# Optimization experiments

Hardware: AMD Instinct MI355X
Metric: run time of the kernel (lower is better)

## Reference

```python
import jax, jax.numpy as jnp
import numpy as np

B, N, E = 32, 128, 16384
D, H, O, A = 72, 72, 72, 4   # n_input, n_hidden, n_output, n_node_attr
C_WEIGHT = 1.0
EPS = 1e-5  # BatchNorm1d default eps


def setup_inputs() -> dict:
    key = jax.random.key(0)
    ks = jax.random.split(key, 16)
    rn = lambda k, shp, s=0.05: jax.random.normal(k, shp, jnp.float32) * s
    return {
        "h": jax.random.normal(ks[0], (B, N, D), jnp.float32),
        "x": jax.random.normal(ks[1], (B, N, 4), jnp.float32),
        "edgei": jax.random.randint(ks[2], (B, E), 0, N),
        "edgej": jax.random.randint(ks[3], (B, E), 0, N),
        "node_attr": jax.random.normal(ks[4], (B, N, A), jnp.float32),
        # phi_e: Linear(2D+2 -> H, no bias), BN, ReLU, Linear(H->H), ReLU
        "We1": rn(ks[5], (2 * D + 2, H)),
        "g1": jnp.ones((H,), jnp.float32), "b1": jnp.zeros((H,), jnp.float32),
        "We2": rn(ks[6], (H, H)), "be2": jnp.zeros((H,), jnp.float32),
        # phi_m: Linear(H->1), Sigmoid
        "Wm": rn(ks[7], (H, 1)), "bm": jnp.zeros((1,), jnp.float32),
        # phi_x: Linear(H->H), ReLU, Linear(H->1, no bias, tiny init)
        "Wx1": rn(ks[8], (H, H)), "bx1": jnp.zeros((H,), jnp.float32),
        "Wx2": rn(ks[9], (H, 1), 0.001),
        # phi_h: Linear(H+D+A -> H), BN, ReLU, Linear(H->O)
        "Wh1": rn(ks[10], (H + D + A, H)), "bh1": jnp.zeros((H,), jnp.float32),
        "gh": jnp.ones((H,), jnp.float32), "bh": jnp.zeros((H,), jnp.float32),
        "Wh2": rn(ks[11], (H, O)), "bh2": jnp.zeros((O,), jnp.float32),
    }


def _psi(p):
    return jnp.sign(p) * jnp.log1p(jnp.abs(p))


def _normsq4(p):  # Minkowski norm: p0^2 - p1^2 - p2^2 - p3^2
    psq = p * p
    return 2.0 * psq[..., 0] - psq.sum(axis=-1)


def _dotsq4(p, q):  # Minkowski inner product
    pq = p * q
    return 2.0 * pq[..., 0] - pq.sum(axis=-1)


def _batchnorm(z, g, b):  # training-mode BatchNorm1d over flattened batch dim
    mu = z.mean(axis=0)
    var = z.var(axis=0)
    return (z - mu) * jax.lax.rsqrt(var + EPS) * g + b


_seg_sum = jax.vmap(lambda d, s: jax.ops.segment_sum(d, s, num_segments=N))


def reference(h, x, edgei, edgej, node_attr,
              We1, g1, b1, We2, be2, Wm, bm,
              Wx1, bx1, Wx2, Wh1, bh1, gh, bh, Wh2, bh2):
    # gather edge endpoint features (equiv. to torch.gather along dim 1)
    xi = jnp.take_along_axis(x, edgei[:, :, None], axis=1)    # [B,E,4]
    xj = jnp.take_along_axis(x, edgej[:, :, None], axis=1)
    hi = jnp.take_along_axis(h, edgei[:, :, None], axis=1)    # [B,E,D]
    hj = jnp.take_along_axis(h, edgej[:, :, None], axis=1)
    x_diff = xi - xj
    norms = _psi(_normsq4(x_diff))[..., None]                 # [B,E,1]
    dots = _psi(_dotsq4(xi, xj))[..., None]                   # [B,E,1]

    # m_model: phi_e then sigmoid gate phi_m
    feat = jnp.concatenate([hi, hj, norms, dots], axis=-1)    # [B,E,2D+2]
    z = feat.reshape(-1, 2 * D + 2) @ We1
    z = jax.nn.relu(_batchnorm(z, g1, b1))
    z = jax.nn.relu(z @ We2 + be2)
    m = z.reshape(B, E, H)
    m = m * jax.nn.sigmoid(m @ Wm + bm)                       # gated messages

    # x_model: equivariant coordinate update (segment mean over edges)
    gate = jax.nn.relu(m @ Wx1 + bx1) @ Wx2                   # [B,E,1]
    trans = jnp.clip(x_diff * gate, -100.0, 100.0)
    agg = _seg_sum(trans, edgei)                              # [B,N,4]
    cnt = _seg_sum(jnp.ones_like(trans), edgei)
    x_out = x + (agg / jnp.maximum(cnt, 1.0)) * C_WEIGHT

    # h_model: segment sum of messages, node MLP, residual
    magg = _seg_sum(m, edgei)                                 # [B,N,H]
    hin = jnp.concatenate([h, magg, node_attr], axis=-1).reshape(-1, H + D + A)
    z2 = hin @ Wh1 + bh1
    z2 = jax.nn.relu(_batchnorm(z2, gh, bh))
    z2 = z2 @ Wh2 + bh2
    h_out = h + z2.reshape(B, N, O)

    return (h_out, x_out, m)
```

## Files before the change

kernel.cpp:

```cpp
#include <hip/hip_runtime.h>

#define BB 32
#define NN 128
#define EE 16384
#define ROWS_E (BB*EE)
#define ROWS_N (BB*NN)
#define EPS_BN 1e-5f

#define XOUT_OFF (ROWS_N*72)
#define M_OFF    (XOUT_OFF + ROWS_N*4)

#define ST1_OFF 0
#define ST2_OFF 512
#define AGG_OFF 1024
#define CNT_OFF (AGG_OFF + ROWS_N*4)
#define MAGG_OFF (CNT_OFF + ROWS_N)
#define Z2_OFF (MAGG_OFF + ROWS_N*72)
#define ZERO_FLOATS Z2_OFF
#define WB_OFF (Z2_OFF + ROWS_N*72)

#define WE1T_OFF 0
#define WE2T_OFF 13440
#define WX1T_OFF 21760
#define WH1T_OFF 30080
#define WH2T_OFF 43520
#define WB_TOTAL 51840

typedef __attribute__((ext_vector_type(8))) short short8;
typedef __attribute__((ext_vector_type(4))) float f32x4;

__device__ __forceinline__ float psi_f(float p) {
    return copysignf(log1pf(fabsf(p)), p);
}
__device__ __forceinline__ unsigned short f2bf(float f) {
    union { float f; unsigned u; } v; v.f = f;
    unsigned r = v.u + 0x7fffu + ((v.u >> 16) & 1u);
    return (unsigned short)(r >> 16);
}
__device__ __forceinline__ unsigned pk(float a, float b) {
    return (unsigned)f2bf(a) | ((unsigned)f2bf(b) << 16);
}

__global__ void k_prep(const float* __restrict__ We1, const float* __restrict__ We2,
                       const float* __restrict__ Wx1, const float* __restrict__ Wh1,
                       const float* __restrict__ Wh2, unsigned short* __restrict__ wb)
{
    int idx = blockIdx.x * 256 + threadIdx.x;
    if (idx >= WB_TOTAL) return;
    const float* src; int off, n, k, K;
    if (idx < WE2T_OFF)      { off = idx;            n = off/168; k = off%168; src = We1; K = 146; }
    else if (idx < WH1T_OFF && idx >= WX1T_OFF) { off = idx - WX1T_OFF; n = off/104; k = off%104; src = Wx1; K = 72; }
    else if (idx < WX1T_OFF) { off = idx - WE2T_OFF; n = off/104; k = off%104; src = We2; K = 72; }
    else if (idx < WH2T_OFF) { off = idx - WH1T_OFF; n = off/168; k = off%168; src = Wh1; K = 148; }
    else                     { off = idx - WH2T_OFF; n = off/104; k = off%104; src = Wh2; K = 72; }
    float v = (n < 72 && k < K) ? src[k * 72 + n] : 0.f;
    wb[idx] = f2bf(v);
}

__global__ __launch_bounds__(256, 4) void k_edge_gemm1(
    const float* __restrict__ h, const float* __restrict__ x,
    const int* __restrict__ ei, const int* __restrict__ ej,
    const unsigned short* __restrict__ We1t, float* __restrict__ z1,
    float* __restrict__ st)
{
    __shared__ unsigned short At[128 * 160];
    int tid = threadIdx.x;
    int rl = tid >> 1, half = tid & 1;
    int row = blockIdx.x * 128 + rl;
    int b = row >> 14;
    int i = ei[row], j = ej[row];
    int node = half ? j : i;
    const float4* hp = (const float4*)(h + (size_t)(b * 128 + node) * 72);
    uint2* arow = (uint2*)(&At[rl * 160 + half * 72]);
    #pragma unroll
    for (int q = 0; q < 18; q++) {
        float4 v = hp[q];
        arow[q] = make_uint2(pk(v.x, v.y), pk(v.z, v.w));
    }
    if (half == 0) {
        float4 xi = *(const float4*)(x + (size_t)(b * 128 + i) * 4);
        float4 xj = *(const float4*)(x + (size_t)(b * 128 + j) * 4);
        float d0 = xi.x - xj.x, d1 = xi.y - xj.y, d2 = xi.z - xj.z, d3 = xi.w - xj.w;
        float nrm = d0*d0 - d1*d1 - d2*d2 - d3*d3;
        float dot = xi.x*xj.x - xi.y*xj.y - xi.z*xj.z - xi.w*xj.w;
        *(unsigned*)(&At[rl * 160 + 144]) = pk(psi_f(nrm), psi_f(dot));
        unsigned* tp = (unsigned*)(&At[rl * 160 + 146]);
        tp[0] = 0u; tp[1] = 0u; tp[2] = 0u;
    } else {
        unsigned* tp = (unsigned*)(&At[rl * 160 + 152]);
        tp[0] = 0u; tp[1] = 0u; tp[2] = 0u; tp[3] = 0u;
    }

    int wv = tid >> 6, lane = tid & 63, c = lane & 15, quad = lane >> 4;
    f32x4 acc[2][5] = {};
    for (int kc = 0; kc < 5; kc++) {
        int k0 = kc * 32 + quad * 8;
        short8 a0 = *(const short8*)(&At[(wv * 32 + c) * 160 + k0]);
        short8 a1 = *(const short8*)(&At[(wv * 32 + 16 + c) * 160 + k0]);
        #pragma unroll
        for (int ct = 0; ct < 5; ct++) {
            short8 bf = *(const short8*)(&We1t[(ct * 16 + c) * 168 + k0]);
            acc[0][ct] = __builtin_amdgcn_mfma_f32_16x16x32_bf16(a0, bf, acc[0][ct], 0, 0, 0);
            acc[1][ct] = __builtin_amdgcn_mfma_f32_16x16x32_bf16(a1, bf, acc[1][ct], 0, 0, 0);
        }
    }
    size_t rbase = (size_t)blockIdx.x * 128 + wv * 32 + quad * 4;
    float* sredw = (float*)(&At[wv * 32 * 160]);
    #pragma unroll
    for (int ct = 0; ct < 5; ct++) {
        int col = ct * 16 + c;
        float s = 0.f, q = 0.f;
        #pragma unroll
        for (int rt = 0; rt < 2; rt++) {
            float* op = z1 + (rbase + rt * 16) * 72 + col;
            #pragma unroll
            for (int r = 0; r < 4; r++) {
                float v = acc[rt][ct][r];
                if (col < 72) op[(size_t)r * 72] = v;
                s += v; q += v * v;
            }
        }
        s += __shfl_xor(s, 16); s += __shfl_xor(s, 32);
        q += __shfl_xor(q, 16); q += __shfl_xor(q, 32);
        if (lane < 16 && col < 72) { sredw[col] = s; sredw[72 + col] = q; }
    }
    __syncthreads();
    if (tid < 144) {
        const float* a = (const float*)At;
        atomicAdd(&st[tid], a[tid] + a[2560 + tid] + a[5120 + tid] + a[7680 + tid]);
    }
}

__global__ void k_finalize(float* __restrict__ st, float inv_rows)
{
    int c = threadIdx.x;
    if (c < 72) {
        float mean = st[c] * inv_rows;
        float var  = st[72 + c] * inv_rows - mean * mean;
        st[144 + c] = mean;
        st[216 + c] = rsqrtf(var + EPS_BN);
    }
}

__global__ __launch_bounds__(256, 6) void k_edge_main(
    const float* __restrict__ x, const int* __restrict__ ei, const int* __restrict__ ej,
    const float* __restrict__ st1, const float* __restrict__ g1, const float* __restrict__ b1,
    const float* __restrict__ be2, const float* __restrict__ Wm, const float* __restrict__ bm,
    const float* __restrict__ bx1, const float* __restrict__ Wx2,
    const unsigned short* __restrict__ We2t, const unsigned short* __restrict__ Wx1t,
    float* __restrict__ m, float* __restrict__ agg, float* __restrict__ cnt)
{
    __shared__ unsigned short Zt[128 * 104];
    __shared__ float g2buf[128];
    int tid = threadIdx.x;
    int rl = tid >> 1, half = tid & 1;
    size_t row = (size_t)blockIdx.x * 128 + rl;
    const float* mean = st1 + 144;
    const float* inv  = st1 + 216;
    const float4* zp = (const float4*)(m + row * 72) + half * 9;
    uint2* arow = (uint2*)(&Zt[rl * 104 + half * 36]);
    #pragma unroll
    for (int q = 0; q < 9; q++) {
        int k = half * 36 + q * 4;
        float4 v = zp[q];
        float a0 = fmaxf((v.x - mean[k  ]) * inv[k  ] * g1[k  ] + b1[k  ], 0.f);
        float a1 = fmaxf((v.y - mean[k+1]) * inv[k+1] * g1[k+1] + b1[k+1], 0.f);
        float a2 = fmaxf((v.z - mean[k+2]) * inv[k+2] * g1[k+2] + b1[k+2], 0.f);
        float a3 = fmaxf((v.w - mean[k+3]) * inv[k+3] * g1[k+3] + b1[k+3], 0.f);
        arow[q] = make_uint2(pk(a0, a1), pk(a2, a3));
    }
    uint2* prow = (uint2*)(&Zt[rl * 104]);
    #pragma unroll
    for (int q = 0; q < 4; q++) prow[18 + half * 4 + q] = make_uint2(0u, 0u);

    int wv = tid >> 6, lane = tid & 63, c = lane & 15, quad = lane >> 4;
    f32x4 acc2[2][5] = {};
    for (int kc = 0; kc < 3; kc++) {
        int k0 = kc * 32 + quad * 8;
        short8 a0 = *(const short8*)(&Zt[(wv * 32 + c) * 104 + k0]);
        short8 a1 = *(const short8*)(&Zt[(wv * 32 + 16 + c) * 104 + k0]);
        #pragma unroll
        for (int ct = 0; ct < 5; ct++) {
            short8 bf = *(const short8*)(&We2t[(ct * 16 + c) * 104 + k0]);
            acc2[0][ct] = __builtin_amdgcn_mfma_f32_16x16x32_bf16(a0, bf, acc2[0][ct], 0, 0, 0);
            acc2[1][ct] = __builtin_amdgcn_mfma_f32_16x16x32_bf16(a1, bf, acc2[1][ct], 0, 0, 0);
        }
    }
    float part[2][4] = {};
    float bm0 = bm[0];
    #pragma unroll
    for (int ct = 0; ct < 5; ct++) {
        int col = ct * 16 + c;
        float bias = (col < 72) ? be2[col] : 0.f;
        float wm   = (col < 72) ? Wm[col]  : 0.f;
        #pragma unroll
        for (int rt = 0; rt < 2; rt++)
            #pragma unroll
            for (int r = 0; r < 4; r++) {
                float t = fmaxf(acc2[rt][ct][r] + bias, 0.f);
                acc2[rt][ct][r] = t;
                part[rt][r] += t * wm;
            }
    }
    float sg[2][4];
    #pragma unroll
    for (int rt = 0; rt < 2; rt++)
        #pragma unroll
        for (int r = 0; r < 4; r++) {
            float s = part[rt][r];
            s += __shfl_xor(s, 1); s += __shfl_xor(s, 2);
            s += __shfl_xor(s, 4); s += __shfl_xor(s, 8);
            sg[rt][r] = 1.f / (1.f + expf(-(s + bm0)));
        }
    size_t rbase = (size_t)blockIdx.x * 128 + wv * 32 + quad * 4;
    #pragma unroll
    for (int rt = 0; rt < 2; rt++)
        #pragma unroll
        for (int ct = 0; ct < 5; ct++) {
            int col = ct * 16 + c;
            #pragma unroll
            for (int r = 0; r < 4; r++) {
                float mv = acc2[rt][ct][r] * sg[rt][r];
                int lrow = wv * 32 + rt * 16 + quad * 4 + r;
                Zt[lrow * 104 + col] = f2bf(mv);
                if (col < 72) m[(rbase + rt * 16 + r) * 72 + col] = mv;
            }
        }
    f32x4 acc3[2][5] = {};
    for (int kc = 0; kc < 3; kc++) {
        int k0 = kc * 32 + quad * 8;
        short8 a0 = *(const short8*)(&Zt[(wv * 32 + c) * 104 + k0]);
        short8 a1 = *(const short8*)(&Zt[(wv * 32 + 16 + c) * 104 + k0]);
        #pragma unroll
        for (int ct = 0; ct < 5; ct++) {
            short8 bf = *(const short8*)(&Wx1t[(ct * 16 + c) * 104 + k0]);
            acc3[0][ct] = __builtin_amdgcn_mfma_f32_16x16x32_bf16(a0, bf, acc3[0][ct], 0, 0, 0);
            acc3[1][ct] = __builtin_amdgcn_mfma_f32_16x16x32_bf16(a1, bf, acc3[1][ct], 0, 0, 0);
        }
    }
    float part3[2][4] = {};
    #pragma unroll
    for (int ct = 0; ct < 5; ct++) {
        int col = ct * 16 + c;
        float bias = (col < 72) ? bx1[col] : 0.f;
        float wx   = (col < 72) ? Wx2[col] : 0.f;
        #pragma unroll
        for (int rt = 0; rt < 2; rt++)
            #pragma unroll
            for (int r = 0; r < 4; r++)
                part3[rt][r] += fmaxf(acc3[rt][ct][r] + bias, 0.f) * wx;
    }
    #pragma unroll
    for (int rt = 0; rt < 2; rt++)
        #pragma unroll
        for (int r = 0; r < 4; r++) {
            float s = part3[rt][r];
            s += __shfl_xor(s, 1); s += __shfl_xor(s, 2);
            s += __shfl_xor(s, 4); s += __shfl_xor(s, 8);
            if (c == 0) g2buf[wv * 32 + rt * 16 + quad * 4 + r] = s;
        }
    __syncthreads();
    if (tid < 128) {
        size_t erow = (size_t)blockIdx.x * 128 + tid;
        int b = (int)(erow >> 14);
        int i2 = ei[erow], j2 = ej[erow];
        float g2 = g2buf[tid];
        float4 xi = *(const float4*)(x + (size_t)(b * 128 + i2) * 4);
        float4 xj = *(const float4*)(x + (size_t)(b * 128 + j2) * 4);
        float t0 = fminf(fmaxf((xi.x - xj.x) * g2, -100.f), 100.f);
        float t1 = fminf(fmaxf((xi.y - xj.y) * g2, -100.f), 100.f);
        float t2 = fminf(fmaxf((xi.z - xj.z) * g2, -100.f), 100.f);
        float t3 = fminf(fmaxf((xi.w - xj.w) * g2, -100.f), 100.f);
        float* ap = agg + (size_t)(b * 128 + i2) * 4;
        atomicAdd(ap + 0, t0); atomicAdd(ap + 1, t1);
        atomicAdd(ap + 2, t2); atomicAdd(ap + 3, t3);
        atomicAdd(cnt + (size_t)(b * 128 + i2), 1.f);
    }
}

__global__ __launch_bounds__(256, 4) void k_magg(
    const float* __restrict__ m, const int* __restrict__ ei, float* __restrict__ magg)
{
    __shared__ float accum[128 * 72];
    int tid = threadIdx.x;
    for (int q = tid; q < 9216; q += 256) accum[q] = 0.f;
    __syncthreads();
    int b = blockIdx.x >> 4, chunk = blockIdx.x & 15;
    int wv = tid >> 6, lane = tid & 63;
    int ebase = b * 16384 + chunk * 1024;
    for (int e = wv; e < 1024; e += 4) {
        int erow = ebase + e;
        int node = ei[erow];
        const float* mr = m + (size_t)erow * 72;
        atomicAdd(&accum[node * 72 + lane], mr[lane]);
        if (lane < 8) atomicAdd(&accum[node * 72 + 64 + lane], mr[64 + lane]);
    }
    __syncthreads();
    float* mg = magg + (size_t)b * 9216;
    for (int q = tid; q < 9216; q += 256) atomicAdd(&mg[q], accum[q]);
}

__global__ __launch_bounds__(256) void k_node_gemm1(
    const float* __restrict__ h, const float* __restrict__ node_attr,
    const float* __restrict__ magg, const unsigned short* __restrict__ Wh1t,
    const float* __restrict__ bh1, float* __restrict__ z2, float* __restrict__ st)
{
    __shared__ unsigned short At[128 * 168];
    __shared__ unsigned short Wt[80 * 168];
    __shared__ float sred[4][144];
    int tid = threadIdx.x;
    {
        const uint4* s = (const uint4*)Wh1t; uint4* d = (uint4*)Wt;
        for (int q = tid; q < 1680; q += 256) d[q] = s[q];
    }
    int rl = tid >> 1, half = tid & 1;
    size_t row = (size_t)blockIdx.x * 128 + rl;
    const float4* sp = (const float4*)((half ? magg : h) + row * 72);
    uint2* arow = (uint2*)(&At[rl * 168 + half * 72]);
    #pragma unroll
    for (int q = 0; q < 18; q++) {
        float4 v = sp[q];
        arow[q] = make_uint2(pk(v.x, v.y), pk(v.z, v.w));
    }
    if (half) {
        float4 na = *(const float4*)(node_attr + row * 4);
        *(unsigned*)(&At[rl * 168 + 144]) = pk(na.x, na.y);
        *(unsigned*)(&At[rl * 168 + 146]) = pk(na.z, na.w);
        unsigned* tailp = (unsigned*)(&At[rl * 168 + 148]);
        #pragma unroll
        for (int q = 0; q < 10; q++) tailp[q] = 0u;
    }
    __syncthreads();

    int wv = tid >> 6, lane = tid & 63, c = lane & 15, quad = lane >> 4;
    f32x4 acc[2][5] = {};
    for (int kc = 0; kc < 5; kc++) {
        int k0 = kc * 32 + quad * 8;
        short8 a0 = *(const short8*)(&At[(wv * 32 + c) * 168 + k0]);
        short8 a1 = *(const short8*)(&At[(wv * 32 + 16 + c) * 168 + k0]);
        #pragma unroll
        for (int ct = 0; ct < 5; ct++) {
            short8 bf = *(const short8*)(&Wt[(ct * 16 + c) * 168 + k0]);
            acc[0][ct] = __builtin_amdgcn_mfma_f32_16x16x32_bf16(a0, bf, acc[0][ct], 0, 0, 0);
            acc[1][ct] = __builtin_amdgcn_mfma_f32_16x16x32_bf16(a1, bf, acc[1][ct], 0, 0, 0);
        }
    }
    size_t rbase = (size_t)blockIdx.x * 128 + wv * 32 + quad * 4;
    #pragma unroll
    for (int ct = 0; ct < 5; ct++) {
        int col = ct * 16 + c;
        float bias = (col < 72) ? bh1[col] : 0.f;
        float s = 0.f, q = 0.f;
        #pragma unroll
        for (int rt = 0; rt < 2; rt++) {
            float* op = z2 + (rbase + rt * 16) * 72 + col;
            #pragma unroll
            for (int r = 0; r < 4; r++) {
                float v = acc[rt][ct][r] + bias;
                if (col < 72) op[(size_t)r * 72] = v;
                s += v; q += v * v;
            }
        }
        s += __shfl_xor(s, 16); s += __shfl_xor(s, 32);
        q += __shfl_xor(q, 16); q += __shfl_xor(q, 32);
        if (lane < 16 && col < 72) { sred[wv][col] = s; sred[wv][72 + col] = q; }
    }
    __syncthreads();
    if (tid < 144)
        atomicAdd(&st[tid], sred[0][tid] + sred[1][tid] + sred[2][tid] + sred[3][tid]);
}

__global__ __launch_bounds__(256) void k_node_final(
    const float* __restrict__ h, const float* __restrict__ x,
    const float* __restrict__ z2, const float* __restrict__ st2,
    const float* __restrict__ gh, const float* __restrict__ bh,
    const unsigned short* __restrict__ Wh2t, const float* __restrict__ bh2,
    const float* __restrict__ agg, const float* __restrict__ cnt,
    float* __restrict__ hout, float* __restrict__ xout)
{
    __shared__ unsigned short Zt[128 * 104];
    __shared__ unsigned short Wt[80 * 104];
    int tid = threadIdx.x;
    {
        const uint4* s = (const uint4*)Wh2t; uint4* d = (uint4*)Wt;
        for (int q = tid; q < 1040; q += 256) d[q] = s[q];
    }
    int rl = tid >> 1, half = tid & 1;
    size_t row = (size_t)blockIdx.x * 128 + rl;
    const float* mean = st2 + 144;
    const float* inv  = st2 + 216;
    const float4* zp = (const float4*)(z2 + row * 72) + half * 9;
    uint2* arow = (uint2*)(&Zt[rl * 104 + half * 36]);
    #pragma unroll
    for (int q = 0; q < 9; q++) {
        int k = half * 36 + q * 4;
        float4 v = zp[q];
        float a0 = fmaxf((v.x - mean[k  ]) * inv[k  ] * gh[k  ] + bh[k  ], 0.f);
        float a1 = fmaxf((v.y - mean[k+1]) * inv[k+1] * gh[k+1] + bh[k+1], 0.f);
        float a2 = fmaxf((v.z - mean[k+2]) * inv[k+2] * gh[k+2] + bh[k+2], 0.f);
        float a3 = fmaxf((v.w - mean[k+3]) * inv[k+3] * gh[k+3] + bh[k+3], 0.f);
        arow[q] = make_uint2(pk(a0, a1), pk(a2, a3));
    }
    uint2* prow = (uint2*)(&Zt[rl * 104]);
    #pragma unroll
    for (int q = 0; q < 4; q++) prow[18 + half * 4 + q] = make_uint2(0u, 0u);
    __syncthreads();

    int wv = tid >> 6, lane = tid & 63, c = lane & 15, quad = lane >> 4;
    f32x4 acc[2][5] = {};
    for (int kc = 0; kc < 3; kc++) {
        int k0 = kc * 32 + quad * 8;
        short8 a0 = *(const short8*)(&Zt[(wv * 32 + c) * 104 + k0]);
        short8 a1 = *(const short8*)(&Zt[(wv * 32 + 16 + c) * 104 + k0]);
        #pragma unroll
        for (int ct = 0; ct < 5; ct++) {
            short8 bf = *(const short8*)(&Wt[(ct * 16 + c) * 104 + k0]);
            acc[0][ct] = __builtin_amdgcn_mfma_f32_16x16x32_bf16(a0, bf, acc[0][ct], 0, 0, 0);
            acc[1][ct] = __builtin_amdgcn_mfma_f32_16x16x32_bf16(a1, bf, acc[1][ct], 0, 0, 0);
        }
    }
    size_t rbase = (size_t)blockIdx.x * 128 + wv * 32 + quad * 4;
    #pragma unroll
    for (int rt = 0; rt < 2; rt++)
        #pragma unroll
        for (int ct = 0; ct < 5; ct++) {
            int col = ct * 16 + c;
            if (col < 72) {
                float bias = bh2[col];
                #pragma unroll
                for (int r = 0; r < 4; r++) {
                    size_t gr = (rbase + rt * 16 + r);
                    hout[gr * 72 + col] = h[gr * 72 + col] + acc[rt][ct][r] + bias;
                }
            }
        }
    if (tid < 128) {
        size_t nrow = (size_t)blockIdx.x * 128 + tid;
        float cn = fmaxf(cnt[nrow], 1.f);
        float4 ag = *(const float4*)(agg + nrow * 4);
        float4 xv = *(const float4*)(x + nrow * 4);
        ((float4*)xout)[nrow] = make_float4(xv.x + ag.x / cn, xv.y + ag.y / cn,
                                            xv.z + ag.z / cn, xv.w + ag.w / cn);
    }
}

extern "C" void kernel_launch(void* const* d_in, const int* in_sizes, int n_in,
                              void* d_out, int out_size, void* d_ws, size_t ws_size,
                              hipStream_t stream)
{
    const float* h   = (const float*)d_in[0];
    const float* x   = (const float*)d_in[1];
    const int*   ei  = (const int*)d_in[2];
    const int*   ej  = (const int*)d_in[3];
    const float* na  = (const float*)d_in[4];
    const float* We1 = (const float*)d_in[5];
    const float* g1  = (const float*)d_in[6];
    const float* b1  = (const float*)d_in[7];
    const float* We2 = (const float*)d_in[8];
    const float* be2 = (const float*)d_in[9];
    const float* Wm  = (const float*)d_in[10];
    const float* bm  = (const float*)d_in[11];
    const float* Wx1 = (const float*)d_in[12];
    const float* bx1 = (const float*)d_in[13];
    const float* Wx2 = (const float*)d_in[14];
    const float* Wh1 = (const float*)d_in[15];
    const float* bh1 = (const float*)d_in[16];
    const float* gh  = (const float*)d_in[17];
    const float* bhp = (const float*)d_in[18];
    const float* Wh2 = (const float*)d_in[19];
    const float* bh2 = (const float*)d_in[20];

    float* out  = (float*)d_out;
    float* hout = out;
    float* xout = out + XOUT_OFF;
    float* m    = out + M_OFF;
    float* ws   = (float*)d_ws;
    float* st1  = ws + ST1_OFF;
    float* st2  = ws + ST2_OFF;
    float* agg  = ws + AGG_OFF;
    float* cnt  = ws + CNT_OFF;
    float* magg = ws + MAGG_OFF;
    float* z2   = ws + Z2_OFF;
    unsigned short* wb = (unsigned short*)(ws + WB_OFF);

    hipMemsetAsync(d_ws, 0, (size_t)ZERO_FLOATS * sizeof(float), stream);
    k_prep<<<(WB_TOTAL + 255) / 256, 256, 0, stream>>>(We1, We2, Wx1, Wh1, Wh2, wb);
    k_edge_gemm1<<<ROWS_E / 128, 256, 0, stream>>>(h, x, ei, ej, wb + WE1T_OFF, m, st1);
    k_finalize<<<1, 128, 0, stream>>>(st1, 1.0f / (float)ROWS_E);
    k_edge_main<<<ROWS_E / 128, 256, 0, stream>>>(x, ei, ej, st1, g1, b1, be2, Wm, bm,
                                                  bx1, Wx2, wb + WE2T_OFF, wb + WX1T_OFF,
                                                  m, agg, cnt);
    k_magg<<<512, 256, 0, stream>>>(m, ei, magg);
    k_node_gemm1<<<ROWS_N / 128, 256, 0, stream>>>(h, na, magg, wb + WH1T_OFF, bh1, z2, st2);
    k_finalize<<<1, 128, 0, stream>>>(st2, 1.0f / (float)ROWS_N);
    k_node_final<<<ROWS_N / 128, 256, 0, stream>>>(h, x, z2, st2, gh, bhp,
                                                   wb + WH2T_OFF, bh2, agg, cnt, hout, xout);
}
```

Measured before the change: 720.9 us.

## Recompute first edge GEMM in fused kernel instead of storing intermediate z1

```diff
diff --git a/kernel.cpp b/kernel.cpp
--- a/kernel.cpp
+++ b/kernel.cpp
@@ -57,16 +57,12 @@
     wb[idx] = f2bf(v);
 }
 
-__global__ __launch_bounds__(256, 4) void k_edge_gemm1(
-    const float* __restrict__ h, const float* __restrict__ x,
-    const int* __restrict__ ei, const int* __restrict__ ej,
-    const unsigned short* __restrict__ We1t, float* __restrict__ z1,
-    float* __restrict__ st)
-{
-    __shared__ unsigned short At[128 * 160];
-    int tid = threadIdx.x;
+__device__ __forceinline__ void stage_feat(
+    unsigned short* At, const float* __restrict__ h, const float* __restrict__ x,
+    const int* __restrict__ ei, const int* __restrict__ ej, int tid, int blk)
+{
     int rl = tid >> 1, half = tid & 1;
-    int row = blockIdx.x * 128 + rl;
+    int row = blk * 128 + rl;
     int b = row >> 14;
     int i = ei[row], j = ej[row];
     int node = half ? j : i;
@@ -90,6 +86,16 @@
         unsigned* tp = (unsigned*)(&At[rl * 160 + 152]);
         tp[0] = 0u; tp[1] = 0u; tp[2] = 0u; tp[3] = 0u;
     }
+}
+
+__global__ __launch_bounds__(256, 4) void k_edge_stats(
+    const float* __restrict__ h, const float* __restrict__ x,
+    const int* __restrict__ ei, const int* __restrict__ ej,
+    const unsigned short* __restrict__ We1t, float* __restrict__ st)
+{
+    __shared__ unsigned short At[128 * 160];
+    int tid = threadIdx.x;
+    stage_feat(At, h, x, ei, ej, tid, blockIdx.x);
 
     int wv = tid >> 6, lane = tid & 63, c = lane & 15, quad = lane >> 4;
     f32x4 acc[2][5] = {};
@@ -104,22 +110,18 @@
             acc[1][ct] = __builtin_amdgcn_mfma_f32_16x16x32_bf16(a1, bf, acc[1][ct], 0, 0, 0);
         }
     }
-    size_t rbase = (size_t)blockIdx.x * 128 + wv * 32 + quad * 4;
     float* sredw = (float*)(&At[wv * 32 * 160]);
     #pragma unroll
     for (int ct = 0; ct < 5; ct++) {
         int col = ct * 16 + c;
         float s = 0.f, q = 0.f;
         #pragma unroll
-        for (int rt = 0; rt < 2; rt++) {
-            float* op = z1 + (rbase + rt * 16) * 72 + col;
+        for (int rt = 0; rt < 2; rt++)
             #pragma unroll
             for (int r = 0; r < 4; r++) {
                 float v = acc[rt][ct][r];
-                if (col < 72) op[(size_t)r * 72] = v;
                 s += v; q += v * v;
             }
-        }
         s += __shfl_xor(s, 16); s += __shfl_xor(s, 32);
         q += __shfl_xor(q, 16); q += __shfl_xor(q, 32);
         if (lane < 16 && col < 72) { sredw[col] = s; sredw[72 + col] = q; }
@@ -142,43 +144,59 @@
     }
 }
 
-__global__ __launch_bounds__(256, 6) void k_edge_main(
-    const float* __restrict__ x, const int* __restrict__ ei, const int* __restrict__ ej,
+__global__ __launch_bounds__(256, 4) void k_edge_fused(
+    const float* __restrict__ h, const float* __restrict__ x,
+    const int* __restrict__ ei, const int* __restrict__ ej,
     const float* __restrict__ st1, const float* __restrict__ g1, const float* __restrict__ b1,
     const float* __restrict__ be2, const float* __restrict__ Wm, const float* __restrict__ bm,
     const float* __restrict__ bx1, const float* __restrict__ Wx2,
-    const unsigned short* __restrict__ We2t, const unsigned short* __restrict__ Wx1t,
+    const unsigned short* __restrict__ We1t, const unsigned short* __restrict__ We2t,
+    const unsigned short* __restrict__ Wx1t,
     float* __restrict__ m, float* __restrict__ agg, float* __restrict__ cnt)
 {
-    __shared__ unsigned short Zt[128 * 104];
-    __shared__ float g2buf[128];
+    __shared__ unsigned short At[128 * 160];
     int tid = threadIdx.x;
-    int rl = tid >> 1, half = tid & 1;
-    size_t row = (size_t)blockIdx.x * 128 + rl;
+    stage_feat(At, h, x, ei, ej, tid, blockIdx.x);
+
+    int wv = tid >> 6, lane = tid & 63, c = lane & 15, quad = lane >> 4;
+    f32x4 acc1[2][5] = {};
+    for (int kc = 0; kc < 5; kc++) {
+        int k0 = kc * 32 + quad * 8;
+        short8 a0 = *(const short8*)(&At[(wv * 32 + c) * 160 + k0]);
+        short8 a1 = *(const short8*)(&At[(wv * 32 + 16 + c) * 160 + k0]);
+        #pragma unroll
+        for (int ct = 0; ct < 5; ct++) {
+            short8 bf = *(const short8*)(&We1t[(ct * 16 + c) * 168 + k0]);
+            acc1[0][ct] = __builtin_amdgcn_mfma_f32_16x16x32_bf16(a0, bf, acc1[0][ct], 0, 0, 0);
+            acc1[1][ct] = __builtin_amdgcn_mfma_f32_16x16x32_bf16(a1, bf, acc1[1][ct], 0, 0, 0);
+        }
+    }
     const float* mean = st1 + 144;
     const float* inv  = st1 + 216;
-    const float4* zp = (const float4*)(m + row * 72) + half * 9;
-    uint2* arow = (uint2*)(&Zt[rl * 104 + half * 36]);
-    #pragma unroll
-    for (int q = 0; q < 9; q++) {
-        int k = half * 36 + q * 4;
-        float4 v = zp[q];
-        float a0 = fmaxf((v.x - mean[k  ]) * inv[k  ] * g1[k  ] + b1[k  ], 0.f);
-        float a1 = fmaxf((v.y - mean[k+1]) * inv[k+1] * g1[k+1] + b1[k+1], 0.f);
-        float a2 = fmaxf((v.z - mean[k+2]) * inv[k+2] * g1[k+2] + b1[k+2], 0.f);
-        float a3 = fmaxf((v.w - mean[k+3]) * inv[k+3] * g1[k+3] + b1[k+3], 0.f);
-        arow[q] = make_uint2(pk(a0, a1), pk(a2, a3));
-    }
-    uint2* prow = (uint2*)(&Zt[rl * 104]);
-    #pragma unroll
-    for (int q = 0; q < 4; q++) prow[18 + half * 4 + q] = make_uint2(0u, 0u);
-
-    int wv = tid >> 6, lane = tid & 63, c = lane & 15, quad = lane >> 4;
+    #pragma unroll
+    for (int ct = 0; ct < 5; ct++) {
+        int col = ct * 16 + c;
+        float mu = 0.f, iv = 0.f, ga = 0.f, be = 0.f;
+        if (col < 72) { mu = mean[col]; iv = inv[col]; ga = g1[col]; be = b1[col]; }
+        #pragma unroll
+        for (int rt = 0; rt < 2; rt++)
+            #pragma unroll
+            for (int r = 0; r < 4; r++) {
+                float a = (col < 72) ? fmaxf((acc1[rt][ct][r] - mu) * iv * ga + be, 0.f) : 0.f;
+                int lrow = wv * 32 + rt * 16 + quad * 4 + r;
+                At[lrow * 160 + col] = f2bf(a);
+            }
+    }
+    {
+        int r_ = lane >> 1, h_ = lane & 1;
+        uint* zp = (uint*)&At[(wv * 32 + r_) * 160 + 80 + h_ * 8];
+        zp[0] = 0u; zp[1] = 0u; zp[2] = 0u; zp[3] = 0u;
+    }
     f32x4 acc2[2][5] = {};
     for (int kc = 0; kc < 3; kc++) {
         int k0 = kc * 32 + quad * 8;
-        short8 a0 = *(const short8*)(&Zt[(wv * 32 + c) * 104 + k0]);
-        short8 a1 = *(const short8*)(&Zt[(wv * 32 + 16 + c) * 104 + k0]);
+        short8 a0 = *(const short8*)(&At[(wv * 32 + c) * 160 + k0]);
+        short8 a1 = *(const short8*)(&At[(wv * 32 + 16 + c) * 160 + k0]);
         #pragma unroll
         for (int ct = 0; ct < 5; ct++) {
             short8 bf = *(const short8*)(&We2t[(ct * 16 + c) * 104 + k0]);
@@ -222,15 +240,15 @@
             for (int r = 0; r < 4; r++) {
                 float mv = acc2[rt][ct][r] * sg[rt][r];
                 int lrow = wv * 32 + rt * 16 + quad * 4 + r;
-                Zt[lrow * 104 + col] = f2bf(mv);
+                At[lrow * 160 + col] = f2bf(mv);
                 if (col < 72) m[(rbase + rt * 16 + r) * 72 + col] = mv;
             }
         }
     f32x4 acc3[2][5] = {};
     for (int kc = 0; kc < 3; kc++) {
         int k0 = kc * 32 + quad * 8;
-        short8 a0 = *(const short8*)(&Zt[(wv * 32 + c) * 104 + k0]);
-        short8 a1 = *(const short8*)(&Zt[(wv * 32 + 16 + c) * 104 + k0]);
+        short8 a0 = *(const short8*)(&At[(wv * 32 + c) * 160 + k0]);
+        short8 a1 = *(const short8*)(&At[(wv * 32 + 16 + c) * 160 + k0]);
         #pragma unroll
         for (int ct = 0; ct < 5; ct++) {
             short8 bf = *(const short8*)(&Wx1t[(ct * 16 + c) * 104 + k0]);
@@ -250,6 +268,7 @@
             for (int r = 0; r < 4; r++)
                 part3[rt][r] += fmaxf(acc3[rt][ct][r] + bias, 0.f) * wx;
     }
+    float* gp = (float*)&At[(wv * 32) * 160 + 96];
     #pragma unroll
     for (int rt = 0; rt < 2; rt++)
         #pragma unroll
@@ -257,14 +276,14 @@
             float s = part3[rt][r];
             s += __shfl_xor(s, 1); s += __shfl_xor(s, 2);
             s += __shfl_xor(s, 4); s += __shfl_xor(s, 8);
-            if (c == 0) g2buf[wv * 32 + rt * 16 + quad * 4 + r] = s;
+            if (c == 0) gp[rt * 16 + quad * 4 + r] = s;
         }
     __syncthreads();
     if (tid < 128) {
         size_t erow = (size_t)blockIdx.x * 128 + tid;
         int b = (int)(erow >> 14);
         int i2 = ei[erow], j2 = ej[erow];
-        float g2 = g2buf[tid];
+        float g2 = *((float*)&At[((tid >> 5) * 32) * 160 + 96] + (tid & 31));
         float4 xi = *(const float4*)(x + (size_t)(b * 128 + i2) * 4);
         float4 xj = *(const float4*)(x + (size_t)(b * 128 + j2) * 4);
         float t0 = fminf(fmaxf((xi.x - xj.x) * g2, -100.f), 100.f);
@@ -285,10 +304,10 @@
     int tid = threadIdx.x;
     for (int q = tid; q < 9216; q += 256) accum[q] = 0.f;
     __syncthreads();
-    int b = blockIdx.x >> 4, chunk = blockIdx.x & 15;
+    int b = blockIdx.x >> 3, chunk = blockIdx.x & 7;
     int wv = tid >> 6, lane = tid & 63;
-    int ebase = b * 16384 + chunk * 1024;
-    for (int e = wv; e < 1024; e += 4) {
+    int ebase = b * 16384 + chunk * 2048;
+    for (int e = wv; e < 2048; e += 4) {
         int erow = ebase + e;
         int node = ei[erow];
         const float* mr = m + (size_t)erow * 72;
@@ -485,12 +504,12 @@
 
     hipMemsetAsync(d_ws, 0, (size_t)ZERO_FLOATS * sizeof(float), stream);
     k_prep<<<(WB_TOTAL + 255) / 256, 256, 0, stream>>>(We1, We2, Wx1, Wh1, Wh2, wb);
-    k_edge_gemm1<<<ROWS_E / 128, 256, 0, stream>>>(h, x, ei, ej, wb + WE1T_OFF, m, st1);
+    k_edge_stats<<<ROWS_E / 128, 256, 0, stream>>>(h, x, ei, ej, wb + WE1T_OFF, st1);
     k_finalize<<<1, 128, 0, stream>>>(st1, 1.0f / (float)ROWS_E);
-    k_edge_main<<<ROWS_E / 128, 256, 0, stream>>>(x, ei, ej, st1, g1, b1, be2, Wm, bm,
-                                                  bx1, Wx2, wb + WE2T_OFF, wb + WX1T_OFF,
-                                                  m, agg, cnt);
-    k_magg<<<512, 256, 0, stream>>>(m, ei, magg);
+    k_edge_fused<<<ROWS_E / 128, 256, 0, stream>>>(h, x, ei, ej, st1, g1, b1, be2, Wm, bm,
+                                                   bx1, Wx2, wb + WE1T_OFF, wb + WE2T_OFF,
+                                                   wb + WX1T_OFF, m, agg, cnt);
+    k_magg<<<256, 256, 0, stream>>>(m, ei, magg);
     k_node_gemm1<<<ROWS_N / 128, 256, 0, stream>>>(h, na, magg, wb + WH1T_OFF, bh1, z2, st2);
     k_finalize<<<1, 128, 0, stream>>>(st2, 1.0f / (float)ROWS_N);
     k_node_final<<<ROWS_N / 128, 256, 0, stream>>>(h, x, z2, st2, gh, bhp,
```

After: 680.1 us. -5.7%, faster.
